# Performance work log

Measured on AMD Instinct MI355X. Metric: run time of the kernel, lower is better.

## Reference

```python
import jax, jax.numpy as jnp
import numpy as np

R = 0.2                 # ball-query radius (Descriptor.r)
MAX_NBRS = 64           # CONFIG['Descriptor']['max_num_neighbors']


def setup_inputs() -> dict:
    key = jax.random.key(0)
    k1, k2, k3, k4, k5, k6 = jax.random.split(key, 6)
    N, F, M = 100000, 64, 2048
    x = jax.random.normal(k1, (N, F), dtype=jnp.float32)
    pos = jax.random.normal(k2, (N, 3), dtype=jnp.float32)
    batch = jnp.sort(jax.random.randint(k3, (N,), 0, 4, dtype=jnp.int64))
    key_idx = jax.random.randint(k4, (M,), 0, N, dtype=jnp.int64)
    # MLP params: Linear(F+3 -> 128), ReLU, Linear(128 -> 128)
    H = 128
    W1 = jax.random.normal(k5, (F + 3, H), dtype=jnp.float32) / np.sqrt(F + 3)
    b1 = jnp.zeros((H,), dtype=jnp.float32)
    W2 = jax.random.normal(k6, (H, H), dtype=jnp.float32) / np.sqrt(H)
    b2 = jnp.zeros((H,), dtype=jnp.float32)
    return {"x": x, "pos": pos, "W1": W1, "b1": b1, "W2": W2, "b2": b2,
            "batch": batch, "key_idx": key_idx}


def reference(x, pos, W1, b1, W2, b2, batch, key_idx):
    N = pos.shape[0]
    qpos = pos[key_idx]            # [M,3]
    qbatch = batch[key_idx]        # [M]

    # Brute-force ball query (what torch-cluster radius does under the hood):
    # squared distances via ||q||^2 + ||p||^2 - 2 q.p  -> [M,N]
    d2 = (jnp.sum(qpos * qpos, -1)[:, None]
          + jnp.sum(pos * pos, -1)[None, :]
          - 2.0 * qpos @ pos.T)
    valid = (d2 <= R * R) & (qbatch[:, None] == batch[None, :])   # [M,N]

    # Take the first MAX_NBRS valid neighbors per query (index order, as PyG).
    order_key = jnp.where(valid, jnp.arange(N)[None, :], N)       # invalid -> N
    neg_vals, idx = jax.lax.top_k(-order_key, MAX_NBRS)           # [M,K]
    valid_k = neg_vals > -N                                       # [M,K] real edge mask

    # PointNetConv message: nn(concat([x_j, pos_j - pos_i])), then max-aggregate.
    x_j = x[idx]                                  # [M,K,F] gather
    rel = pos[idx] - qpos[:, None, :]             # [M,K,3]
    h = jnp.concatenate([x_j, rel], axis=-1)      # [M,K,F+3]
    h = jax.nn.relu(h @ W1 + b1)
    h = h @ W2 + b2                               # [M,K,H]
    h = jnp.where(valid_k[..., None], h, -jnp.inf)
    out = jnp.max(h, axis=1)                      # [M,H] max-scatter
    out = jnp.where(jnp.any(valid_k, axis=1)[:, None], out, 0.0)

    # F.normalize(out, dim=-1)
    out = out / jnp.maximum(jnp.linalg.norm(out, axis=-1, keepdims=True), 1e-12)
    return out
```

## Files before the change

kernel.cpp:

```cpp
#include <hip/hip_runtime.h>
#include <math.h>

#define MAXK 64
#define HDIM 128
#define FDIM 64
#define NB 4
#define QG 16
#define S  64

typedef __attribute__((ext_vector_type(8))) short bf16x8;
typedef __attribute__((ext_vector_type(4))) float f32x4;

__device__ __forceinline__ unsigned short f2bf(float f) {
    unsigned x = __float_as_uint(f);
    unsigned r = (x + 0x7fffu + ((x >> 16) & 1u)) >> 16;
    return (unsigned short)r;
}
__device__ __forceinline__ unsigned pk2(float a, float b) {
    return (unsigned)f2bf(a) | ((unsigned)f2bf(b) << 16);
}

__global__ __launch_bounds__(256) void prep_kernel(
    const float* __restrict__ W1, const float* __restrict__ W2,
    const int* __restrict__ batch, const int* __restrict__ key_idx,
    int N, int M,
    unsigned short* __restrict__ W1bf, unsigned short* __restrict__ W2bf,
    int* __restrict__ bounds, int* __restrict__ qn, int* __restrict__ qlist)
{
    int tid = threadIdx.x;
    if (blockIdx.x == 0) {
        __shared__ int wcnt[4][NB];
        __shared__ int base[NB];
        int lane = tid & 63, w = tid >> 6;
        if (tid < NB) base[tid] = 0;
        __syncthreads();
        int nchunk = (M + 255) / 256;
        for (int c = 0; c < nchunk; ++c) {
            int i = c*256 + tid;
            int qb = (i < M) ? batch[key_idx[i]] : -1;
            unsigned long long m0 = __ballot(qb == 0);
            unsigned long long m1 = __ballot(qb == 1);
            unsigned long long m2 = __ballot(qb == 2);
            unsigned long long m3 = __ballot(qb == 3);
            if (lane == 0) {
                wcnt[w][0] = (int)__popcll(m0); wcnt[w][1] = (int)__popcll(m1);
                wcnt[w][2] = (int)__popcll(m2); wcnt[w][3] = (int)__popcll(m3);
            }
            __syncthreads();
            if (qb >= 0) {
                unsigned long long mym = (qb == 0) ? m0 : (qb == 1) ? m1
                                        : (qb == 2) ? m2 : m3;
                int off = 0;
                for (int ww = 0; ww < 4; ++ww)
                    if (ww < w) off += wcnt[ww][qb];
                int slot = base[qb] + off
                         + (int)__popcll(mym & ((1ull << lane) - 1ull));
                qlist[qb*M + slot] = i;
            }
            __syncthreads();
            if (tid < NB) {
                int t2 = 0;
                for (int ww = 0; ww < 4; ++ww) t2 += wcnt[ww][tid];
                base[tid] += t2;
            }
            __syncthreads();
        }
        if (tid < NB) qn[tid] = base[tid];
    } else if (blockIdx.x == 1) {
        if (tid <= NB) {
            int v = tid, a = 0, e = N;
            while (a < e) { int mid = (a+e) >> 1; if (batch[mid] < v) a = mid+1; else e = mid; }
            bounds[v] = a;
        }
    } else {
        int s = (blockIdx.x - 2)*256 + tid;
        if (s < 1536) {
            int cb = s / 192, rem = s % 192, ks = rem / 64, lane = rem % 64;
            int col = cb*16 + (lane & 15);
            int k0  = ks*32 + (lane >> 4)*8;
            unsigned short v[8];
            #pragma unroll
            for (int j = 0; j < 8; ++j) {
                int k = k0 + j;
                v[j] = (k < 67) ? f2bf(W1[k*HDIM + col]) : (unsigned short)0;
            }
            uint4 p;
            p.x = (unsigned)v[0] | ((unsigned)v[1] << 16);
            p.y = (unsigned)v[2] | ((unsigned)v[3] << 16);
            p.z = (unsigned)v[4] | ((unsigned)v[5] << 16);
            p.w = (unsigned)v[6] | ((unsigned)v[7] << 16);
            *reinterpret_cast<uint4*>(&W1bf[(size_t)s*8]) = p;
        } else if (s < 3584) {
            int s2 = s - 1536;
            int cb = s2 >> 8, ks = (s2 >> 6) & 3, lane = s2 & 63;
            int col = cb*16 + (lane & 15);
            int k0  = ks*32 + (lane >> 4)*8;
            unsigned short v[8];
            #pragma unroll
            for (int j = 0; j < 8; ++j) v[j] = f2bf(W2[(k0+j)*HDIM + col]);
            uint4 p;
            p.x = (unsigned)v[0] | ((unsigned)v[1] << 16);
            p.y = (unsigned)v[2] | ((unsigned)v[3] << 16);
            p.z = (unsigned)v[4] | ((unsigned)v[5] << 16);
            p.w = (unsigned)v[6] | ((unsigned)v[7] << 16);
            *reinterpret_cast<uint4*>(&W2bf[(size_t)s2*8]) = p;
        }
    }
}

__global__ __launch_bounds__(256) void scan_kernel(
    const float* __restrict__ pos, const int* __restrict__ key_idx,
    const int* __restrict__ bounds, const int* __restrict__ qn,
    const int* __restrict__ qlist, int M,
    int* __restrict__ lists, int* __restrict__ lcnt)
{
    __shared__ __align__(16) float4 qtile[4][QG];
    __shared__ int qid_s[4][QG];

    int w = threadIdx.x >> 6, lane = threadIdx.x & 63;
    int unit = blockIdx.x*4 + w;
    int qgidx = unit >> 6, s = unit & (S-1);

    int n0 = qn[0], n1 = qn[1], n2 = qn[2], n3 = qn[3];
    int g0 = (n0+QG-1)/QG, g1 = (n1+QG-1)/QG, g2 = (n2+QG-1)/QG;
    int g3 = (n3+QG-1)/QG;
    int bb, g, nq;
    if      (qgidx < g0)          { bb = 0; g = qgidx;          nq = n0; }
    else if (qgidx < g0+g1)       { bb = 1; g = qgidx-g0;       nq = n1; }
    else if (qgidx < g0+g1+g2)    { bb = 2; g = qgidx-g0-g1;    nq = n2; }
    else if (qgidx < g0+g1+g2+g3) { bb = 3; g = qgidx-g0-g1-g2; nq = n3; }
    else return;

    if (lane < QG) {
        int qs = g*QG + lane;
        int me = (qs < nq) ? qlist[bb*M + qs] : -1;
        qid_s[w][lane] = me;
        float4 qv = make_float4(0.f, 0.f, 0.f, 0.f);
        if (me >= 0) {
            int qi = key_idx[me];
            float qx = pos[3*qi+0], qy = pos[3*qi+1], qz = pos[3*qi+2];
            float q2 = __fadd_rn(__fadd_rn(__fmul_rn(qx,qx), __fmul_rn(qy,qy)), __fmul_rn(qz,qz));
            qv = make_float4(qx, qy, qz, q2);
        }
        qtile[w][lane] = qv;
    }
    float4 qr[QG]; int qidr[QG];
    #pragma unroll
    for (int t = 0; t < QG; ++t) { qr[t] = qtile[w][t]; qidr[t] = qid_s[w][t]; }

    int lo = bounds[bb], hi = bounds[bb+1];
    int seg  = hi - lo;
    int slen = (seg + S - 1) >> 6;
    int start = lo + s*slen;
    int send  = min(start + slen, hi);

    const float R2 = 0.04f;

    int lc[QG];
    #pragma unroll
    for (int t = 0; t < QG; ++t) lc[t] = (qidr[t] >= 0) ? 0 : MAXK;

    unsigned long long lmask_lt = (1ull << lane) - 1ull;

    for (int base = start; base < send; base += 64) {
        int j = base + lane;
        float px, py, pz, pw;
        if (j < send) {
            px = pos[3*j+0]; py = pos[3*j+1]; pz = pos[3*j+2];
            pw = __fadd_rn(__fadd_rn(__fmul_rn(px,px), __fmul_rn(py,py)), __fmul_rn(pz,pz));
        } else {
            px = 0.f; py = 0.f; pz = 0.f; pw = INFINITY;
        }
        #pragma unroll
        for (int t = 0; t < QG; ++t) {
            float4 q = qr[t];
            float dt = __fadd_rn(__fadd_rn(__fmul_rn(q.x,px), __fmul_rn(q.y,py)), __fmul_rn(q.z,pz));
            float d2 = __fsub_rn(__fadd_rn(q.w, pw), __fmul_rn(2.0f, dt));
            bool hit = (d2 <= R2);
            unsigned long long mask = __ballot(hit);
            if (mask) {
                if (hit && lc[t] < MAXK) {
                    int slot = lc[t] + (int)__popcll(mask & lmask_lt);
                    if (slot < MAXK)
                        lists[(qidr[t]*S + s)*MAXK + slot] = j;
                }
                lc[t] += (int)__popcll(mask);
            }
        }
    }
    #pragma unroll
    for (int t = 0; t < QG; ++t) {
        if (lane == t && qidr[t] >= 0)
            lcnt[qidr[t]*S + s] = min(lc[t], MAXK);
    }
}

__global__ __launch_bounds__(256) void mlp_kernel(
    const float* __restrict__ x, const float* __restrict__ pos,
    const unsigned short* __restrict__ W1bf, const unsigned short* __restrict__ W2bf,
    const float* __restrict__ b1, const float* __restrict__ b2,
    const int* __restrict__ key_idx,
    const int* __restrict__ lists, const int* __restrict__ lcnt,
    float* __restrict__ out, int M)
{
    __shared__ __align__(16) unsigned short h_lds[4*16*128];
    __shared__ float pmax_s[4][HDIM];
    __shared__ float rsum[2];

    int m   = blockIdx.x;
    int tid = threadIdx.x;
    int lane = tid & 63, w = tid >> 6;
    int colq = lane & 15, rq = lane >> 4;

    int qi = key_idx[m];
    float qx = pos[3*qi+0], qy = pos[3*qi+1], qz = pos[3*qi+2];

    int ct = lcnt[m*S + lane];
    int pre = ct;
    #pragma unroll
    for (int o = 1; o < 64; o <<= 1) {
        int v = __shfl_up(pre, o, 64);
        if (lane >= o) pre += v;
    }
    int excl = pre - ct;
    int total = __shfl(pre, 63, 64);
    int cnt = min(total, MAXK);

    int row = w*16 + colq;
    int sp = 0;
    #pragma unroll
    for (int st = 32; st >= 1; st >>= 1) {
        int cand = sp + st;
        int e = __shfl(excl, (cand < 64) ? cand : 63, 64);
        if (cand < 64 && e <= row) sp = cand;
    }
    int off = row - __shfl(excl, sp, 64);
    int src = (m*S + sp)*MAXK + off;

    union { bf16x8 v; uint4 u; } A0, A1, A2;
    A0.u = make_uint4(0,0,0,0); A1.u = A0.u; A2.u = A0.u;
    if (row < cnt) {
        int idx = lists[src];
        const float4* xp = reinterpret_cast<const float4*>(x + (size_t)idx*FDIM + rq*8);
        float4 u0 = xp[0], u1 = xp[1];
        const float4* xq = reinterpret_cast<const float4*>(x + (size_t)idx*FDIM + 32 + rq*8);
        float4 u2 = xq[0], u3 = xq[1];
        A0.u.x = pk2(u0.x, u0.y); A0.u.y = pk2(u0.z, u0.w);
        A0.u.z = pk2(u1.x, u1.y); A0.u.w = pk2(u1.z, u1.w);
        A1.u.x = pk2(u2.x, u2.y); A1.u.y = pk2(u2.z, u2.w);
        A1.u.z = pk2(u3.x, u3.y); A1.u.w = pk2(u3.z, u3.w);
        if (rq == 0) {
            float p0 = pos[3*idx+0], p1 = pos[3*idx+1], p2v = pos[3*idx+2];
            A2.u.x = pk2(p0 - qx, p1 - qy);
            A2.u.y = pk2(p2v - qz, 0.f);
        }
    }

    const bf16x8* W1f = reinterpret_cast<const bf16x8*>(W1bf);
    const bf16x8* W2f = reinterpret_cast<const bf16x8*>(W2bf);

    #pragma unroll
    for (int cb = 0; cb < 8; ++cb) {
        f32x4 c = {0.f, 0.f, 0.f, 0.f};
        c = __builtin_amdgcn_mfma_f32_16x16x32_bf16(A0.v, W1f[(cb*3+0)*64 + lane], c, 0, 0, 0);
        c = __builtin_amdgcn_mfma_f32_16x16x32_bf16(A1.v, W1f[(cb*3+1)*64 + lane], c, 0, 0, 0);
        c = __builtin_amdgcn_mfma_f32_16x16x32_bf16(A2.v, W1f[(cb*3+2)*64 + lane], c, 0, 0, 0);
        int col = cb*16 + colq;
        float bias = b1[col];
        #pragma unroll
        for (int reg = 0; reg < 4; ++reg) {
            int r = rq*4 + reg;
            float h = fmaxf(c[reg] + bias, 0.f);
            h_lds[w*2048 + r*128 + (col ^ ((r & 7) << 3))] = f2bf(h);
        }
    }

    int r = colq, swz = (r & 7) << 3;
    bf16x8 g0 = *reinterpret_cast<const bf16x8*>(&h_lds[w*2048 + r*128 + ((  0 + rq*8) ^ swz)]);
    bf16x8 g1 = *reinterpret_cast<const bf16x8*>(&h_lds[w*2048 + r*128 + (( 32 + rq*8) ^ swz)]);
    bf16x8 g2 = *reinterpret_cast<const bf16x8*>(&h_lds[w*2048 + r*128 + (( 64 + rq*8) ^ swz)]);
    bf16x8 g3 = *reinterpret_cast<const bf16x8*>(&h_lds[w*2048 + r*128 + (( 96 + rq*8) ^ swz)]);
    #pragma unroll
    for (int cb = 0; cb < 8; ++cb) {
        f32x4 c = {0.f, 0.f, 0.f, 0.f};
        c = __builtin_amdgcn_mfma_f32_16x16x32_bf16(g0, W2f[(cb*4+0)*64 + lane], c, 0, 0, 0);
        c = __builtin_amdgcn_mfma_f32_16x16x32_bf16(g1, W2f[(cb*4+1)*64 + lane], c, 0, 0, 0);
        c = __builtin_amdgcn_mfma_f32_16x16x32_bf16(g2, W2f[(cb*4+2)*64 + lane], c, 0, 0, 0);
        c = __builtin_amdgcn_mfma_f32_16x16x32_bf16(g3, W2f[(cb*4+3)*64 + lane], c, 0, 0, 0);
        int col = cb*16 + colq;
        float bias = b2[col];
        float mx = -INFINITY;
        #pragma unroll
        for (int reg = 0; reg < 4; ++reg) {
            int rr = w*16 + rq*4 + reg;
            float val = c[reg] + bias;
            if (rr < cnt) mx = fmaxf(mx, val);
        }
        mx = fmaxf(mx, __shfl_xor(mx, 16, 64));
        mx = fmaxf(mx, __shfl_xor(mx, 32, 64));
        if (rq == 0) pmax_s[w][col] = mx;
    }
    __syncthreads();

    int c = tid & 127, g = tid >> 7;
    float v = fmaxf(fmaxf(pmax_s[0][c], pmax_s[1][c]),
                    fmaxf(pmax_s[2][c], pmax_s[3][c]));
    if (cnt == 0) v = 0.f;
    float sacc = (g == 0) ? v*v : 0.f;
    #pragma unroll
    for (int o = 32; o > 0; o >>= 1) sacc += __shfl_xor(sacc, o, 64);
    if (g == 0 && (tid & 63) == 0) rsum[tid >> 6] = sacc;
    __syncthreads();
    if (g == 0) {
        float nrm = fmaxf(sqrtf(rsum[0] + rsum[1]), 1e-12f);
        out[(size_t)m*HDIM + c] = v / nrm;
    }
}

extern "C" void kernel_launch(void* const* d_in, const int* in_sizes, int n_in,
                              void* d_out, int out_size, void* d_ws, size_t ws_size,
                              hipStream_t stream)
{
    const float* x       = (const float*)d_in[0];
    const float* pos     = (const float*)d_in[1];
    const float* W1      = (const float*)d_in[2];
    const float* b1      = (const float*)d_in[3];
    const float* W2      = (const float*)d_in[4];
    const float* b2      = (const float*)d_in[5];
    const int*   batch   = (const int*)d_in[6];
    const int*   key_idx = (const int*)d_in[7];

    int N = in_sizes[6];
    int M = in_sizes[7];

    unsigned short* W1bf = (unsigned short*)d_ws;
    unsigned short* W2bf = W1bf + 12288;
    int* bounds   = (int*)(W2bf + 16384);
    int* qn       = bounds + 8;
    int* qlist    = qn + 8;
    int* lists    = qlist + (size_t)NB * M;
    int* lcnt     = lists + (size_t)M * S * MAXK;

    prep_kernel<<<16, 256, 0, stream>>>(W1, W2, batch, key_idx, N, M,
                                        W1bf, W2bf, bounds, qn, qlist);

    int max_units = (M/QG + NB) * S;
    scan_kernel<<<(max_units + 3)/4, 256, 0, stream>>>(
        pos, key_idx, bounds, qn, qlist, M, lists, lcnt);

    mlp_kernel<<<M, 256, 0, stream>>>(x, pos, W1bf, W2bf, b1, b2, key_idx,
                                      lists, lcnt, (float*)d_out, M);
}
```

Baseline: 139.8 us.

## Process four queries per MLP block with weights staged in shared memory

Each MLP block now handles four queries instead of one and copies the bf16 W1/W2 weights into LDS once, so all four queries reuse them. The neighbour x/pos gathers for all four queries are issued up front, so their latencies overlap before the MFMA work starts. This trades more LDS per block (about 56KB) and more registers, which lowers occupancy, for fewer global weight reads and better hiding of gather latency. The grid shrinks to M/4 blocks, which assumes M is divisible by 4.

```diff
diff --git a/kernel.cpp b/kernel.cpp
--- a/kernel.cpp
+++ b/kernel.cpp
@@ -7,6 +7,7 @@
 #define NB 4
 #define QG 16
 #define S  64
+#define NQ 4
 
 typedef __attribute__((ext_vector_type(8))) short bf16x8;
 typedef __attribute__((ext_vector_type(4))) float f32x4;
@@ -203,117 +204,148 @@
     const int* __restrict__ lists, const int* __restrict__ lcnt,
     float* __restrict__ out, int M)
 {
+    __shared__ __align__(16) unsigned short w_lds[28672];
     __shared__ __align__(16) unsigned short h_lds[4*16*128];
     __shared__ float pmax_s[4][HDIM];
     __shared__ float rsum[2];
 
-    int m   = blockIdx.x;
     int tid = threadIdx.x;
     int lane = tid & 63, w = tid >> 6;
     int colq = lane & 15, rq = lane >> 4;
-
-    int qi = key_idx[m];
-    float qx = pos[3*qi+0], qy = pos[3*qi+1], qz = pos[3*qi+2];
-
-    int ct = lcnt[m*S + lane];
-    int pre = ct;
-    #pragma unroll
-    for (int o = 1; o < 64; o <<= 1) {
-        int v = __shfl_up(pre, o, 64);
-        if (lane >= o) pre += v;
-    }
-    int excl = pre - ct;
-    int total = __shfl(pre, 63, 64);
-    int cnt = min(total, MAXK);
-
     int row = w*16 + colq;
-    int sp = 0;
-    #pragma unroll
-    for (int st = 32; st >= 1; st >>= 1) {
-        int cand = sp + st;
-        int e = __shfl(excl, (cand < 64) ? cand : 63, 64);
-        if (cand < 64 && e <= row) sp = cand;
-    }
-    int off = row - __shfl(excl, sp, 64);
-    int src = (m*S + sp)*MAXK + off;
-
-    union { bf16x8 v; uint4 u; } A0, A1, A2;
-    A0.u = make_uint4(0,0,0,0); A1.u = A0.u; A2.u = A0.u;
-    if (row < cnt) {
-        int idx = lists[src];
-        const float4* xp = reinterpret_cast<const float4*>(x + (size_t)idx*FDIM + rq*8);
-        float4 u0 = xp[0], u1 = xp[1];
-        const float4* xq = reinterpret_cast<const float4*>(x + (size_t)idx*FDIM + 32 + rq*8);
-        float4 u2 = xq[0], u3 = xq[1];
-        A0.u.x = pk2(u0.x, u0.y); A0.u.y = pk2(u0.z, u0.w);
-        A0.u.z = pk2(u1.x, u1.y); A0.u.w = pk2(u1.z, u1.w);
-        A1.u.x = pk2(u2.x, u2.y); A1.u.y = pk2(u2.z, u2.w);
-        A1.u.z = pk2(u3.x, u3.y); A1.u.w = pk2(u3.z, u3.w);
-        if (rq == 0) {
-            float p0 = pos[3*idx+0], p1 = pos[3*idx+1], p2v = pos[3*idx+2];
-            A2.u.x = pk2(p0 - qx, p1 - qy);
-            A2.u.y = pk2(p2v - qz, 0.f);
-        }
-    }
-
-    const bf16x8* W1f = reinterpret_cast<const bf16x8*>(W1bf);
-    const bf16x8* W2f = reinterpret_cast<const bf16x8*>(W2bf);
-
-    #pragma unroll
-    for (int cb = 0; cb < 8; ++cb) {
-        f32x4 c = {0.f, 0.f, 0.f, 0.f};
-        c = __builtin_amdgcn_mfma_f32_16x16x32_bf16(A0.v, W1f[(cb*3+0)*64 + lane], c, 0, 0, 0);
-        c = __builtin_amdgcn_mfma_f32_16x16x32_bf16(A1.v, W1f[(cb*3+1)*64 + lane], c, 0, 0, 0);
-        c = __builtin_amdgcn_mfma_f32_16x16x32_bf16(A2.v, W1f[(cb*3+2)*64 + lane], c, 0, 0, 0);
-        int col = cb*16 + colq;
-        float bias = b1[col];
-        #pragma unroll
-        for (int reg = 0; reg < 4; ++reg) {
-            int r = rq*4 + reg;
-            float h = fmaxf(c[reg] + bias, 0.f);
-            h_lds[w*2048 + r*128 + (col ^ ((r & 7) << 3))] = f2bf(h);
-        }
-    }
-
-    int r = colq, swz = (r & 7) << 3;
-    bf16x8 g0 = *reinterpret_cast<const bf16x8*>(&h_lds[w*2048 + r*128 + ((  0 + rq*8) ^ swz)]);
-    bf16x8 g1 = *reinterpret_cast<const bf16x8*>(&h_lds[w*2048 + r*128 + (( 32 + rq*8) ^ swz)]);
-    bf16x8 g2 = *reinterpret_cast<const bf16x8*>(&h_lds[w*2048 + r*128 + (( 64 + rq*8) ^ swz)]);
-    bf16x8 g3 = *reinterpret_cast<const bf16x8*>(&h_lds[w*2048 + r*128 + (( 96 + rq*8) ^ swz)]);
-    #pragma unroll
-    for (int cb = 0; cb < 8; ++cb) {
-        f32x4 c = {0.f, 0.f, 0.f, 0.f};
-        c = __builtin_amdgcn_mfma_f32_16x16x32_bf16(g0, W2f[(cb*4+0)*64 + lane], c, 0, 0, 0);
-        c = __builtin_amdgcn_mfma_f32_16x16x32_bf16(g1, W2f[(cb*4+1)*64 + lane], c, 0, 0, 0);
-        c = __builtin_amdgcn_mfma_f32_16x16x32_bf16(g2, W2f[(cb*4+2)*64 + lane], c, 0, 0, 0);
-        c = __builtin_amdgcn_mfma_f32_16x16x32_bf16(g3, W2f[(cb*4+3)*64 + lane], c, 0, 0, 0);
-        int col = cb*16 + colq;
-        float bias = b2[col];
-        float mx = -INFINITY;
-        #pragma unroll
-        for (int reg = 0; reg < 4; ++reg) {
-            int rr = w*16 + rq*4 + reg;
-            float val = c[reg] + bias;
-            if (rr < cnt) mx = fmaxf(mx, val);
-        }
-        mx = fmaxf(mx, __shfl_xor(mx, 16, 64));
-        mx = fmaxf(mx, __shfl_xor(mx, 32, 64));
-        if (rq == 0) pmax_s[w][col] = mx;
+    int m0 = blockIdx.x * NQ;
+
+    {
+        const uint4* s1 = reinterpret_cast<const uint4*>(W1bf);
+        const uint4* s2 = reinterpret_cast<const uint4*>(W2bf);
+        uint4* d = reinterpret_cast<uint4*>(w_lds);
+        #pragma unroll
+        for (int i = 0; i < 6; ++i) d[tid + i*256] = s1[tid + i*256];
+        #pragma unroll
+        for (int i = 0; i < 8; ++i) d[1536 + tid + i*256] = s2[tid + i*256];
+    }
+
+    int cnts[NQ];
+    float4 xa[NQ], xb[NQ], xc[NQ], xd[NQ];
+    float relx[NQ], rely[NQ], relz[NQ];
+    #pragma unroll
+    for (int qq = 0; qq < NQ; ++qq) {
+        int m = m0 + qq;
+        int ct = lcnt[m*S + lane];
+        int pre = ct;
+        #pragma unroll
+        for (int o = 1; o < 64; o <<= 1) {
+            int v = __shfl_up(pre, o, 64);
+            if (lane >= o) pre += v;
+        }
+        int excl = pre - ct;
+        int total = __shfl(pre, 63, 64);
+        int cnt = min(total, MAXK);
+        int sp = 0;
+        #pragma unroll
+        for (int st = 32; st >= 1; st >>= 1) {
+            int cand = sp + st;
+            int e = __shfl(excl, (cand < 64) ? cand : 63, 64);
+            if (cand < 64 && e <= row) sp = cand;
+        }
+        int off = row - __shfl(excl, sp, 64);
+        cnts[qq] = cnt;
+        xa[qq] = make_float4(0,0,0,0); xb[qq] = xa[qq];
+        xc[qq] = xa[qq]; xd[qq] = xa[qq];
+        relx[qq] = 0.f; rely[qq] = 0.f; relz[qq] = 0.f;
+        if (row < cnt) {
+            int idx = lists[(m*S + sp)*MAXK + off];
+            const float4* xp = reinterpret_cast<const float4*>(x + (size_t)idx*FDIM + rq*8);
+            xa[qq] = xp[0]; xb[qq] = xp[1];
+            const float4* xq2 = reinterpret_cast<const float4*>(x + (size_t)idx*FDIM + 32 + rq*8);
+            xc[qq] = xq2[0]; xd[qq] = xq2[1];
+            if (rq == 0) {
+                int qi = key_idx[m];
+                relx[qq] = pos[3*idx+0] - pos[3*qi+0];
+                rely[qq] = pos[3*idx+1] - pos[3*qi+1];
+                relz[qq] = pos[3*idx+2] - pos[3*qi+2];
+            }
+        }
     }
     __syncthreads();
 
-    int c = tid & 127, g = tid >> 7;
-    float v = fmaxf(fmaxf(pmax_s[0][c], pmax_s[1][c]),
-                    fmaxf(pmax_s[2][c], pmax_s[3][c]));
-    if (cnt == 0) v = 0.f;
-    float sacc = (g == 0) ? v*v : 0.f;
-    #pragma unroll
-    for (int o = 32; o > 0; o >>= 1) sacc += __shfl_xor(sacc, o, 64);
-    if (g == 0 && (tid & 63) == 0) rsum[tid >> 6] = sacc;
-    __syncthreads();
-    if (g == 0) {
-        float nrm = fmaxf(sqrtf(rsum[0] + rsum[1]), 1e-12f);
-        out[(size_t)m*HDIM + c] = v / nrm;
+    const bf16x8* W1f = reinterpret_cast<const bf16x8*>(w_lds);
+    const bf16x8* W2f = reinterpret_cast<const bf16x8*>(w_lds + 12288);
+
+    #pragma unroll
+    for (int qq = 0; qq < NQ; ++qq) {
+        int m = m0 + qq;
+        int cnt = cnts[qq];
+
+        union { bf16x8 v; uint4 u; } A0, A1, A2;
+        A0.u = make_uint4(0,0,0,0); A1.u = A0.u; A2.u = A0.u;
+        if (row < cnt) {
+            A0.u.x = pk2(xa[qq].x, xa[qq].y); A0.u.y = pk2(xa[qq].z, xa[qq].w);
+            A0.u.z = pk2(xb[qq].x, xb[qq].y); A0.u.w = pk2(xb[qq].z, xb[qq].w);
+            A1.u.x = pk2(xc[qq].x, xc[qq].y); A1.u.y = pk2(xc[qq].z, xc[qq].w);
+            A1.u.z = pk2(xd[qq].x, xd[qq].y); A1.u.w = pk2(xd[qq].z, xd[qq].w);
+            if (rq == 0) {
+                A2.u.x = pk2(relx[qq], rely[qq]);
+                A2.u.y = pk2(relz[qq], 0.f);
+            }
+        }
+
+        #pragma unroll
+        for (int cb = 0; cb < 8; ++cb) {
+            f32x4 c = {0.f, 0.f, 0.f, 0.f};
+            c = __builtin_amdgcn_mfma_f32_16x16x32_bf16(A0.v, W1f[(cb*3+0)*64 + lane], c, 0, 0, 0);
+            c = __builtin_amdgcn_mfma_f32_16x16x32_bf16(A1.v, W1f[(cb*3+1)*64 + lane], c, 0, 0, 0);
+            c = __builtin_amdgcn_mfma_f32_16x16x32_bf16(A2.v, W1f[(cb*3+2)*64 + lane], c, 0, 0, 0);
+            int col = cb*16 + colq;
+            float bias = b1[col];
+            #pragma unroll
+            for (int reg = 0; reg < 4; ++reg) {
+                int r = rq*4 + reg;
+                float h = fmaxf(c[reg] + bias, 0.f);
+                h_lds[w*2048 + r*128 + (col ^ ((r & 7) << 3))] = f2bf(h);
+            }
+        }
+
+        int r = colq, swz = (r & 7) << 3;
+        bf16x8 g0 = *reinterpret_cast<const bf16x8*>(&h_lds[w*2048 + r*128 + ((  0 + rq*8) ^ swz)]);
+        bf16x8 g1 = *reinterpret_cast<const bf16x8*>(&h_lds[w*2048 + r*128 + (( 32 + rq*8) ^ swz)]);
+        bf16x8 g2 = *reinterpret_cast<const bf16x8*>(&h_lds[w*2048 + r*128 + (( 64 + rq*8) ^ swz)]);
+        bf16x8 g3 = *reinterpret_cast<const bf16x8*>(&h_lds[w*2048 + r*128 + (( 96 + rq*8) ^ swz)]);
+        #pragma unroll
+        for (int cb = 0; cb < 8; ++cb) {
+            f32x4 c = {0.f, 0.f, 0.f, 0.f};
+            c = __builtin_amdgcn_mfma_f32_16x16x32_bf16(g0, W2f[(cb*4+0)*64 + lane], c, 0, 0, 0);
+            c = __builtin_amdgcn_mfma_f32_16x16x32_bf16(g1, W2f[(cb*4+1)*64 + lane], c, 0, 0, 0);
+            c = __builtin_amdgcn_mfma_f32_16x16x32_bf16(g2, W2f[(cb*4+2)*64 + lane], c, 0, 0, 0);
+            c = __builtin_amdgcn_mfma_f32_16x16x32_bf16(g3, W2f[(cb*4+3)*64 + lane], c, 0, 0, 0);
+            int col = cb*16 + colq;
+            float bias = b2[col];
+            float mx = -INFINITY;
+            #pragma unroll
+            for (int reg = 0; reg < 4; ++reg) {
+                int rr = w*16 + rq*4 + reg;
+                float val = c[reg] + bias;
+                if (rr < cnt) mx = fmaxf(mx, val);
+            }
+            mx = fmaxf(mx, __shfl_xor(mx, 16, 64));
+            mx = fmaxf(mx, __shfl_xor(mx, 32, 64));
+            if (rq == 0) pmax_s[w][col] = mx;
+        }
+        __syncthreads();
+
+        int c = tid & 127, g = tid >> 7;
+        float v = fmaxf(fmaxf(pmax_s[0][c], pmax_s[1][c]),
+                        fmaxf(pmax_s[2][c], pmax_s[3][c]));
+        if (cnt == 0) v = 0.f;
+        float sacc = (g == 0) ? v*v : 0.f;
+        #pragma unroll
+        for (int o = 32; o > 0; o >>= 1) sacc += __shfl_xor(sacc, o, 64);
+        if (g == 0 && (tid & 63) == 0) rsum[tid >> 6] = sacc;
+        __syncthreads();
+        if (g == 0) {
+            float nrm = fmaxf(sqrtf(rsum[0] + rsum[1]), 1e-12f);
+            out[(size_t)m*HDIM + c] = v / nrm;
+        }
     }
 }
 
@@ -348,6 +380,6 @@
     scan_kernel<<<(max_units + 3)/4, 256, 0, stream>>>(
         pos, key_idx, bounds, qn, qlist, M, lists, lcnt);
 
-    mlp_kernel<<<M, 256, 0, stream>>>(x, pos, W1bf, W2bf, b1, b2, key_idx,
-                                      lists, lcnt, (float*)d_out, M);
-}
+    mlp_kernel<<<M/NQ, 256, 0, stream>>>(x, pos, W1bf, W2bf, b1, b2, key_idx,
+                                         lists, lcnt, (float*)d_out, M);
+}
```

Measured after the change: 139.2 us. No clear change (-0.5%).
